# Kernel tuning notes

Hardware: AMD Instinct MI355X
Metric: run time of the kernel (lower is better)

The kernel has to match this reference:

```python
import jax, jax.numpy as jnp
import numpy as np

N = 262144   # nodes per plane
B = 64       # events per batch
C = 5        # semantic classes
D = 64       # node_features
E = 3        # event classes


def _softmax_aggr(x, idx, t):
    """PyG SoftmaxAggregation: w = segment_softmax(t*x), out = segment_sum(w*x).
    x: [N, F] float, idx: [N] int segment ids, t: [1] learnable temperature."""
    s = t * x                                               # [N, F]
    m = jax.ops.segment_max(s, idx, num_segments=B)         # [B, F]
    m = jnp.where(jnp.isfinite(m), m, jnp.zeros_like(m))    # guard empty segments
    e = jnp.exp(s - m[idx])                                 # [N, F]
    denom = jax.ops.segment_sum(e, idx, num_segments=B)     # [B, F]
    w = e / denom[idx]                                      # [N, F]
    return jax.ops.segment_sum(w * x, idx, num_segments=B)  # [B, F]


def setup_inputs() -> dict:
    key = jax.random.key(0)
    ks = jax.random.split(key, 8)
    inp = {}
    for i, p in enumerate(['u', 'v', 'y']):
        inp[f'm_{p}'] = jax.random.normal(ks[i], (N, C, D), dtype=jnp.float32)
        inp[f'batch_{p}'] = jnp.sort(jax.random.randint(ks[3 + i], (N,), 0, B))
        inp[f't_{p}'] = jnp.ones((1,), dtype=jnp.float32)
    inp['W'] = jax.random.normal(ks[6], (E, 3 * C * D), dtype=jnp.float32) * 0.02
    inp['b'] = jnp.zeros((E,), dtype=jnp.float32)
    return inp


def reference(m_u, m_v, m_y, batch_u, batch_v, batch_y, t_u, t_v, t_y, W, b):
    xs = []
    for m, idx, t in ((m_u, batch_u, t_u), (m_v, batch_v, t_v), (m_y, batch_y, t_y)):
        x = m.reshape(m.shape[0], -1)          # flatten(1): [N, C*D]
        xs.append(_softmax_aggr(x, idx, t))    # [B, C*D]
    feat = jnp.concatenate(xs, axis=-1)        # [B, 3*C*D]
    return feat @ W.T + b                      # [B, E]
```

## Files before the change

### kernel.cpp

```cpp
#include <hip/hip_runtime.h>
#include <math.h>

#define NNODES 262144
#define BATCH  64
#define CD     320
#define NPLANE 3
#define NCHUNK 8
#define TY     8
#define NEG_BIG (-3.0e38f)

__device__ __forceinline__ int lower_bound_dev(const int* __restrict__ a, int n, int key) {
    int lo = 0, hi = n;
    while (lo < hi) {
        int mid = (lo + hi) >> 1;
        if (a[mid] < key) lo = mid + 1; else hi = mid;
    }
    return lo;
}

__device__ __forceinline__ void combine_state(float& m, float& d, float& n,
                                              float m2, float d2, float n2) {
    float M  = fmaxf(m, m2);
    float p  = __expf(-fabsf(m - m2));
    bool  ge = (m >= m2);
    float s1 = ge ? 1.0f : p;
    float s2 = ge ? p : 1.0f;
    d = d * s1 + d2 * s2;
    n = n * s1 + n2 * s2;
    m = M;
}

__global__ __launch_bounds__(512)
void seg_softmax_partial(const float* __restrict__ m_u, const int* __restrict__ b_u, const float* __restrict__ t_u,
                         const float* __restrict__ m_v, const int* __restrict__ b_v, const float* __restrict__ t_v,
                         const float* __restrict__ m_y, const int* __restrict__ b_y, const float* __restrict__ t_y,
                         float* __restrict__ part)
{
    const int c     = blockIdx.x;
    const int bseg  = blockIdx.y;
    const int plane = blockIdx.z;

    const float* x; const int* idx; float tval;
    if (plane == 0)      { x = m_u; idx = b_u; tval = t_u[0]; }
    else if (plane == 1) { x = m_v; idx = b_v; tval = t_v[0]; }
    else                 { x = m_y; idx = b_y; tval = t_y[0]; }

    const int start = lower_bound_dev(idx, NNODES, bseg);
    const int end   = lower_bound_dev(idx, NNODES, bseg + 1);

    const int tx = threadIdx.x;
    const int ty = threadIdx.y;

    float m[5], d[5], n[5];
    #pragma unroll
    for (int j = 0; j < 5; ++j) { m[j] = NEG_BIG; d[j] = 0.f; n[j] = 0.f; }

    for (int i = start + c * TY + ty; i < end; i += NCHUNK * TY) {
        const float* row = x + (size_t)i * CD + tx;
        float xv[5];
        #pragma unroll
        for (int j = 0; j < 5; ++j) xv[j] = row[j * 64];
        #pragma unroll
        for (int j = 0; j < 5; ++j) {
            float s  = tval * xv[j];
            float p  = __expf(-fabsf(s - m[j]));
            bool  gt = (s > m[j]);
            float scale = gt ? p : 1.0f;
            float e     = gt ? 1.0f : p;
            m[j] = fmaxf(m[j], s);
            d[j] = d[j] * scale + e;
            n[j] = n[j] * scale + e * xv[j];
        }
    }

    __shared__ float sm[TY][CD];
    __shared__ float sd[TY][CD];
    __shared__ float sn[TY][CD];
    #pragma unroll
    for (int j = 0; j < 5; ++j) {
        sm[ty][tx + 64 * j] = m[j];
        sd[ty][tx + 64 * j] = d[j];
        sn[ty][tx + 64 * j] = n[j];
    }
    __syncthreads();

    const int lin = ty * 64 + tx;
    if (lin < CD) {
        float M = sm[0][lin], D = sd[0][lin], Nn = sn[0][lin];
        #pragma unroll
        for (int r = 1; r < TY; ++r)
            combine_state(M, D, Nn, sm[r][lin], sd[r][lin], sn[r][lin]);
        size_t base = ((((size_t)plane * BATCH + bseg) * NCHUNK + c) * 3) * CD + lin;
        part[base]          = M;
        part[base + CD]     = D;
        part[base + 2 * CD] = Nn;
    }
}

__global__ __launch_bounds__(CD)
void merge_feat(const float* __restrict__ part, float* __restrict__ feat)
{
    const int f     = threadIdx.x;
    const int bseg  = blockIdx.x;
    const int plane = blockIdx.y;

    size_t base = ((((size_t)plane * BATCH + bseg) * NCHUNK) * 3) * CD + f;
    float M = part[base], D = part[base + CD], Nn = part[base + 2 * CD];
    #pragma unroll
    for (int cidx = 1; cidx < NCHUNK; ++cidx) {
        size_t b2 = base + (size_t)cidx * 3 * CD;
        combine_state(M, D, Nn, part[b2], part[b2 + CD], part[b2 + 2 * CD]);
    }
    float out = (D > 0.f) ? (Nn / D) : 0.f;
    feat[(size_t)bseg * (NPLANE * CD) + plane * CD + f] = out;
}

__global__ __launch_bounds__(192)
void decode_out(const float* __restrict__ feat, const float* __restrict__ W,
                const float* __restrict__ bias, float* __restrict__ out)
{
    const int tid  = threadIdx.x;
    const int bseg = tid / 3;
    const int e    = tid % 3;
    const float4* fr = (const float4*)(feat + (size_t)bseg * (NPLANE * CD));
    const float4* wr = (const float4*)(W    + (size_t)e    * (NPLANE * CD));
    float a0 = 0.f, a1 = 0.f, a2 = 0.f, a3 = 0.f;
    #pragma unroll 4
    for (int q = 0; q < (NPLANE * CD) / 16; ++q) {
        float4 f0 = fr[4 * q + 0], w0 = wr[4 * q + 0];
        float4 f1 = fr[4 * q + 1], w1 = wr[4 * q + 1];
        float4 f2 = fr[4 * q + 2], w2 = wr[4 * q + 2];
        float4 f3 = fr[4 * q + 3], w3 = wr[4 * q + 3];
        a0 += f0.x * w0.x + f0.y * w0.y + f0.z * w0.z + f0.w * w0.w;
        a1 += f1.x * w1.x + f1.y * w1.y + f1.z * w1.z + f1.w * w1.w;
        a2 += f2.x * w2.x + f2.y * w2.y + f2.z * w2.z + f2.w * w2.w;
        a3 += f3.x * w3.x + f3.y * w3.y + f3.z * w3.z + f3.w * w3.w;
    }
    out[tid] = (a0 + a1) + (a2 + a3) + bias[e];
}

extern "C" void kernel_launch(void* const* d_in, const int* in_sizes, int n_in,
                              void* d_out, int out_size, void* d_ws, size_t ws_size,
                              hipStream_t stream)
{
    const float* m_u = (const float*)d_in[0];
    const int*   b_u = (const int*)  d_in[1];
    const float* t_u = (const float*)d_in[2];
    const float* m_v = (const float*)d_in[3];
    const int*   b_v = (const int*)  d_in[4];
    const float* t_v = (const float*)d_in[5];
    const float* m_y = (const float*)d_in[6];
    const int*   b_y = (const int*)  d_in[7];
    const float* t_y = (const float*)d_in[8];
    const float* W   = (const float*)d_in[9];
    const float* bia = (const float*)d_in[10];
    float* out = (float*)d_out;

    float* part = (float*)d_ws;
    float* feat = part + (size_t)NPLANE * BATCH * NCHUNK * 3 * CD;

    dim3 g1(NCHUNK, BATCH, NPLANE), b1(64, TY);
    seg_softmax_partial<<<g1, b1, 0, stream>>>(m_u, b_u, t_u, m_v, b_v, t_v,
                                               m_y, b_y, t_y, part);

    dim3 g2(BATCH, NPLANE), b2(CD);
    merge_feat<<<g2, b2, 0, stream>>>(part, feat);

    decode_out<<<1, 192, 0, stream>>>(feat, W, bia, out);
}
```

Baseline: 867.5 us.

## Vectorize row loads as float4 with prefetch and fuse merge with decode

The main kernel now assigns each thread a float4 of features, 80 threads per row and 4 rows per block (320 threads instead of 512). Each thread software-prefetches the next row's float4 while updating the online-softmax state of the current one. The merge and decode kernels are combined into one kernel that reduces the per-block dot products with wave shuffles, which removes one launch and the feat buffer round-trip. Fewer rows are in flight per block, so latency hiding depends on the prefetch and on occupancy.

```diff
diff --git a/kernel.cpp b/kernel.cpp
--- a/kernel.cpp
+++ b/kernel.cpp
@@ -6,7 +6,9 @@
 #define CD     320
 #define NPLANE 3
 #define NCHUNK 8
-#define TY     8
+#define RSLOT  4
+#define NQ     (CD / 4)
+#define BLK1   (RSLOT * NQ)
 #define NEG_BIG (-3.0e38f)
 
 __device__ __forceinline__ int lower_bound_dev(const int* __restrict__ a, int n, int key) {
@@ -30,7 +32,19 @@
     m = M;
 }
 
-__global__ __launch_bounds__(512)
+__device__ __forceinline__ void update_state(float& m, float& d, float& n,
+                                             float xv, float tval) {
+    float s  = tval * xv;
+    float p  = __expf(-fabsf(s - m));
+    bool  gt = (s > m);
+    float scale = gt ? p : 1.0f;
+    float e     = gt ? 1.0f : p;
+    m = fmaxf(m, s);
+    d = d * scale + e;
+    n = n * scale + e * xv;
+}
+
+__global__ __launch_bounds__(BLK1)
 void seg_softmax_partial(const float* __restrict__ m_u, const int* __restrict__ b_u, const float* __restrict__ t_u,
                          const float* __restrict__ m_v, const int* __restrict__ b_v, const float* __restrict__ t_v,
                          const float* __restrict__ m_y, const int* __restrict__ b_y, const float* __restrict__ t_y,
@@ -48,95 +62,92 @@
     const int start = lower_bound_dev(idx, NNODES, bseg);
     const int end   = lower_bound_dev(idx, NNODES, bseg + 1);
 
-    const int tx = threadIdx.x;
-    const int ty = threadIdx.y;
+    const int tid = threadIdx.x;
+    const int q   = tid % NQ;
+    const int r   = tid / NQ;
 
-    float m[5], d[5], n[5];
+    float m[4], d[4], n[4];
     #pragma unroll
-    for (int j = 0; j < 5; ++j) { m[j] = NEG_BIG; d[j] = 0.f; n[j] = 0.f; }
+    for (int j = 0; j < 4; ++j) { m[j] = NEG_BIG; d[j] = 0.f; n[j] = 0.f; }
 
-    for (int i = start + c * TY + ty; i < end; i += NCHUNK * TY) {
-        const float* row = x + (size_t)i * CD + tx;
-        float xv[5];
-        #pragma unroll
-        for (int j = 0; j < 5; ++j) xv[j] = row[j * 64];
-        #pragma unroll
-        for (int j = 0; j < 5; ++j) {
-            float s  = tval * xv[j];
-            float p  = __expf(-fabsf(s - m[j]));
-            bool  gt = (s > m[j]);
-            float scale = gt ? p : 1.0f;
-            float e     = gt ? 1.0f : p;
-            m[j] = fmaxf(m[j], s);
-            d[j] = d[j] * scale + e;
-            n[j] = n[j] * scale + e * xv[j];
+    const int stride = NCHUNK * RSLOT;
+    const int i0 = start + c * RSLOT + r;
+    const float4* __restrict__ xp = (const float4*)x;
+
+    if (i0 < end) {
+        float4 cur = xp[(size_t)i0 * NQ + q];
+        for (int i = i0; i < end; i += stride) {
+            const int inext  = i + stride;
+            const int iclamp = (inext < end) ? inext : (end - 1);
+            float4 nxt = xp[(size_t)iclamp * NQ + q];
+            update_state(m[0], d[0], n[0], cur.x, tval);
+            update_state(m[1], d[1], n[1], cur.y, tval);
+            update_state(m[2], d[2], n[2], cur.z, tval);
+            update_state(m[3], d[3], n[3], cur.w, tval);
+            cur = nxt;
         }
     }
 
-    __shared__ float sm[TY][CD];
-    __shared__ float sd[TY][CD];
-    __shared__ float sn[TY][CD];
-    #pragma unroll
-    for (int j = 0; j < 5; ++j) {
-        sm[ty][tx + 64 * j] = m[j];
-        sd[ty][tx + 64 * j] = d[j];
-        sn[ty][tx + 64 * j] = n[j];
-    }
+    __shared__ float sm[RSLOT * CD];
+    __shared__ float sd[RSLOT * CD];
+    __shared__ float sn[RSLOT * CD];
+    const int wbase = r * CD + 4 * q;
+    *(float4*)&sm[wbase] = make_float4(m[0], m[1], m[2], m[3]);
+    *(float4*)&sd[wbase] = make_float4(d[0], d[1], d[2], d[3]);
+    *(float4*)&sn[wbase] = make_float4(n[0], n[1], n[2], n[3]);
     __syncthreads();
 
-    const int lin = ty * 64 + tx;
-    if (lin < CD) {
-        float M = sm[0][lin], D = sd[0][lin], Nn = sn[0][lin];
-        #pragma unroll
-        for (int r = 1; r < TY; ++r)
-            combine_state(M, D, Nn, sm[r][lin], sd[r][lin], sn[r][lin]);
-        size_t base = ((((size_t)plane * BATCH + bseg) * NCHUNK + c) * 3) * CD + lin;
-        part[base]          = M;
-        part[base + CD]     = D;
-        part[base + 2 * CD] = Nn;
-    }
+    const int f = tid;
+    float M = sm[f], D = sd[f], Nn = sn[f];
+    #pragma unroll
+    for (int rr = 1; rr < RSLOT; ++rr)
+        combine_state(M, D, Nn, sm[rr * CD + f], sd[rr * CD + f], sn[rr * CD + f]);
+
+    size_t base = ((((size_t)plane * BATCH + bseg) * NCHUNK + c) * 3) * CD + f;
+    part[base]          = M;
+    part[base + CD]     = D;
+    part[base + 2 * CD] = Nn;
 }
 
 __global__ __launch_bounds__(CD)
-void merge_feat(const float* __restrict__ part, float* __restrict__ feat)
+void merge_decode(const float* __restrict__ part, const float* __restrict__ W,
+                  const float* __restrict__ bias, float* __restrict__ out)
 {
-    const int f     = threadIdx.x;
-    const int bseg  = blockIdx.x;
-    const int plane = blockIdx.y;
+    const int b = blockIdx.x;
+    const int f = threadIdx.x;
 
-    size_t base = ((((size_t)plane * BATCH + bseg) * NCHUNK) * 3) * CD + f;
-    float M = part[base], D = part[base + CD], Nn = part[base + 2 * CD];
+    float acc0 = 0.f, acc1 = 0.f, acc2 = 0.f;
     #pragma unroll
-    for (int cidx = 1; cidx < NCHUNK; ++cidx) {
-        size_t b2 = base + (size_t)cidx * 3 * CD;
-        combine_state(M, D, Nn, part[b2], part[b2 + CD], part[b2 + 2 * CD]);
+    for (int p = 0; p < NPLANE; ++p) {
+        size_t base = ((((size_t)p * BATCH + b) * NCHUNK) * 3) * CD + f;
+        float M = part[base], D = part[base + CD], Nn = part[base + 2 * CD];
+        #pragma unroll
+        for (int cidx = 1; cidx < NCHUNK; ++cidx) {
+            size_t b2 = base + (size_t)cidx * 3 * CD;
+            combine_state(M, D, Nn, part[b2], part[b2 + CD], part[b2 + 2 * CD]);
+        }
+        float fv = (D > 0.f) ? (Nn / D) : 0.f;
+        acc0 += fv * W[0 * (NPLANE * CD) + p * CD + f];
+        acc1 += fv * W[1 * (NPLANE * CD) + p * CD + f];
+        acc2 += fv * W[2 * (NPLANE * CD) + p * CD + f];
     }
-    float out = (D > 0.f) ? (Nn / D) : 0.f;
-    feat[(size_t)bseg * (NPLANE * CD) + plane * CD + f] = out;
-}
 
-__global__ __launch_bounds__(192)
-void decode_out(const float* __restrict__ feat, const float* __restrict__ W,
-                const float* __restrict__ bias, float* __restrict__ out)
-{
-    const int tid  = threadIdx.x;
-    const int bseg = tid / 3;
-    const int e    = tid % 3;
-    const float4* fr = (const float4*)(feat + (size_t)bseg * (NPLANE * CD));
-    const float4* wr = (const float4*)(W    + (size_t)e    * (NPLANE * CD));
-    float a0 = 0.f, a1 = 0.f, a2 = 0.f, a3 = 0.f;
-    #pragma unroll 4
-    for (int q = 0; q < (NPLANE * CD) / 16; ++q) {
-        float4 f0 = fr[4 * q + 0], w0 = wr[4 * q + 0];
-        float4 f1 = fr[4 * q + 1], w1 = wr[4 * q + 1];
-        float4 f2 = fr[4 * q + 2], w2 = wr[4 * q + 2];
-        float4 f3 = fr[4 * q + 3], w3 = wr[4 * q + 3];
-        a0 += f0.x * w0.x + f0.y * w0.y + f0.z * w0.z + f0.w * w0.w;
-        a1 += f1.x * w1.x + f1.y * w1.y + f1.z * w1.z + f1.w * w1.w;
-        a2 += f2.x * w2.x + f2.y * w2.y + f2.z * w2.z + f2.w * w2.w;
-        a3 += f3.x * w3.x + f3.y * w3.y + f3.z * w3.z + f3.w * w3.w;
+    #pragma unroll
+    for (int off = 32; off > 0; off >>= 1) {
+        acc0 += __shfl_down(acc0, off);
+        acc1 += __shfl_down(acc1, off);
+        acc2 += __shfl_down(acc2, off);
     }
-    out[tid] = (a0 + a1) + (a2 + a3) + bias[e];
+    __shared__ float red[BLK1 / 64][3];
+    const int wave = f >> 6, lane = f & 63;
+    if (lane == 0) { red[wave][0] = acc0; red[wave][1] = acc1; red[wave][2] = acc2; }
+    __syncthreads();
+    if (f < 3) {
+        float s = bias[f];
+        #pragma unroll
+        for (int w = 0; w < CD / 64; ++w) s += red[w][f];
+        out[b * 3 + f] = s;
+    }
 }
 
 extern "C" void kernel_launch(void* const* d_in, const int* in_sizes, int n_in,
@@ -157,14 +168,10 @@
     float* out = (float*)d_out;
 
     float* part = (float*)d_ws;
-    float* feat = part + (size_t)NPLANE * BATCH * NCHUNK * 3 * CD;
 
-    dim3 g1(NCHUNK, BATCH, NPLANE), b1(64, TY);
+    dim3 g1(NCHUNK, BATCH, NPLANE), b1(BLK1);
     seg_softmax_partial<<<g1, b1, 0, stream>>>(m_u, b_u, t_u, m_v, b_v, t_v,
                                                m_y, b_y, t_y, part);
 
-    dim3 g2(BATCH, NPLANE), b2(CD);
-    merge_feat<<<g2, b2, 0, stream>>>(part, feat);
-
-    decode_out<<<1, 192, 0, stream>>>(feat, W, bia, out);
+    merge_decode<<<BATCH, CD, 0, stream>>>(part, W, bia, out);
 }
```

Measured after the change: 875.6 us. Within noise of the previous version (+0.9%).
